# Kernel tuning notes

Hardware: AMD Instinct MI355X
Metric: run time of the kernel (lower is better)

The kernel has to match this reference:

```python
import jax, jax.numpy as jnp
import numpy as np

EPS = 1e-5

def conv3d(x, w, b):
    y = jax.lax.conv_general_dilated(x, w, (1, 1, 1), [(1, 1), (1, 1), (1, 1)],
                                     dimension_numbers=('NCDHW', 'OIDHW', 'NCDHW'))
    return y + b[None, :, None, None, None]

def batchnorm(x, g, b):
    # training-mode BN: biased batch statistics over (N, D, H, W)
    m = jnp.mean(x, axis=(0, 2, 3, 4), keepdims=True)
    v = jnp.mean((x - m) ** 2, axis=(0, 2, 3, 4), keepdims=True)
    return (x - m) * jax.lax.rsqrt(v + EPS) * g[None, :, None, None, None] + b[None, :, None, None, None]

def deform_conv3d(x, offset, w, b):
    # x: (B,C,D,H,W); offset: (B, 3*27, D,H,W); w: (O,C,3,3,3)
    B, C, D, H, W = x.shape
    N = 27
    xp = jnp.pad(x, ((0, 0), (0, 0), (1, 1), (1, 1), (1, 1)))
    Dp, Hp, Wp = D + 2, H + 2, W + 2
    off = offset.reshape(B, 3, N, D, H, W)
    kk = jnp.arange(3, dtype=x.dtype) - 1.0  # kernel taps -1,0,1
    kd, kh, kw = [a.reshape(-1) for a in jnp.meshgrid(kk, kk, kk, indexing='ij')]
    # sampling positions in padded coords: p0 (=out idx + pad) + kernel tap + learned offset
    pd = jnp.clip((jnp.arange(D, dtype=x.dtype) + 1.0)[None, None, :, None, None]
                  + kd[None, :, None, None, None] + off[:, 0], 0.0, Dp - 1)
    ph = jnp.clip((jnp.arange(H, dtype=x.dtype) + 1.0)[None, None, None, :, None]
                  + kh[None, :, None, None, None] + off[:, 1], 0.0, Hp - 1)
    pw = jnp.clip((jnp.arange(W, dtype=x.dtype) + 1.0)[None, None, None, None, :]
                  + kw[None, :, None, None, None] + off[:, 2], 0.0, Wp - 1)
    q0d = jnp.clip(jnp.floor(pd), 0, Dp - 2); td = jnp.clip(pd - q0d, 0.0, 1.0)
    q0h = jnp.clip(jnp.floor(ph), 0, Hp - 2); th = jnp.clip(ph - q0h, 0.0, 1.0)
    q0w = jnp.clip(jnp.floor(pw), 0, Wp - 2); tw = jnp.clip(pw - q0w, 0.0, 1.0)
    q0d = q0d.astype(jnp.int32); q0h = q0h.astype(jnp.int32); q0w = q0w.astype(jnp.int32)
    xf = xp.reshape(B, C, -1)
    acc = jnp.zeros((B, C, N, D, H, W), dtype=x.dtype)
    for i in (0, 1):
        for j in (0, 1):
            for k in (0, 1):
                idx = ((q0d + i) * Hp + (q0h + j)) * Wp + (q0w + k)  # (B,N,D,H,W)
                g = ((td if i else 1.0 - td) * (th if j else 1.0 - th) * (tw if k else 1.0 - tw))
                gath = jnp.take_along_axis(xf, idx.reshape(B, 1, -1), axis=2).reshape(B, C, N, D, H, W)
                acc = acc + g[:, None] * gath
    out = jnp.einsum('bcndhw,ocn->bodhw', acc, w.reshape(w.shape[0], C, N))
    return out + b[None, :, None, None, None]


def setup_inputs() -> dict:
    ks = jax.random.split(jax.random.key(0), 16)
    s = 0.05
    f32 = jnp.float32
    return {
        'x': jax.random.normal(ks[0], (4, 1, 28, 28, 8), f32),
        'c1w': jax.random.normal(ks[1], (32, 1, 3, 3, 3), f32) * s, 'c1b': jnp.zeros((32,), f32),
        'g1': jnp.ones((32,), f32), 'b1': jnp.zeros((32,), f32),
        'c2w': jax.random.normal(ks[2], (64, 32, 3, 3, 3), f32) * s, 'c2b': jnp.zeros((64,), f32),
        'g2': jnp.ones((64,), f32), 'b2': jnp.zeros((64,), f32),
        'c3w': jax.random.normal(ks[3], (128, 64, 3, 3, 3), f32) * s, 'c3b': jnp.zeros((128,), f32),
        'g3': jnp.ones((128,), f32), 'b3': jnp.zeros((128,), f32),
        'ow': jax.random.normal(ks[4], (81, 128, 3, 3, 3), f32) * s, 'ob': jnp.zeros((81,), f32),
        'dw': jax.random.normal(ks[5], (128, 128, 3, 3, 3), f32) * s, 'db': jnp.zeros((128,), f32),
        'g4': jnp.ones((128,), f32), 'b4': jnp.zeros((128,), f32),
        'fcw': jax.random.normal(ks[6], (10, 128), f32) * s, 'fcb': jnp.zeros((10,), f32),
    }


def reference(x, c1w, c1b, g1, b1, c2w, c2b, g2, b2, c3w, c3b, g3, b3,
              ow, ob, dw, db, g4, b4, fcw, fcb):
    h = batchnorm(jax.nn.relu(conv3d(x, c1w, c1b)), g1, b1)
    h = batchnorm(jax.nn.relu(conv3d(h, c2w, c2b)), g2, b2)
    h = batchnorm(jax.nn.relu(conv3d(h, c3w, c3b)), g3, b3)
    offsets = conv3d(h, ow, ob)
    h = batchnorm(jax.nn.relu(deform_conv3d(h, offsets, dw, db)), g4, b4)
    pooled = jnp.mean(h, axis=(2, 3, 4))  # avg_pool over full (28,28,d) extent
    logits = pooled @ fcw.T + fcb
    return jax.nn.log_softmax(logits, axis=1), offsets
```

## Files before the change

kernel.cpp:

```cpp
#include <hip/hip_runtime.h>
#include <hip/hip_bf16.h>
#include <math.h>

#define BB 4
#define SP 6272
#define NSP 25088
#define EPS 1e-5f

typedef unsigned short u16;
typedef __attribute__((ext_vector_type(8))) short v8s;
typedef __attribute__((ext_vector_type(4))) float v4f;

__device__ __forceinline__ u16 f2b(float f) {
    unsigned u = __float_as_uint(f);
    return (u16)((u + 0x7fffu + ((u >> 16) & 1u)) >> 16);
}
__device__ __forceinline__ float b2f(u16 s) {
    return __uint_as_float(((unsigned)s) << 16);
}
__device__ __forceinline__ float b2f_lo(unsigned x) { return __uint_as_float(x << 16); }
__device__ __forceinline__ float b2f_hi(unsigned x) { return __uint_as_float(x & 0xffff0000u); }
__device__ __forceinline__ unsigned pk2(float a, float b) {
    __hip_bfloat162 h = __float22bfloat162_rn(make_float2(a, b));
    unsigned u;
    __builtin_memcpy(&u, &h, 4);
    return u;
}

__global__ __launch_bounds__(256) void prepack_all(const float* __restrict__ c2w,
        const float* __restrict__ c3w, const float* __restrict__ ow,
        const float* __restrict__ dw, u16* __restrict__ wpk2,
        u16* __restrict__ wpk3, u16* __restrict__ wpko, u16* __restrict__ dwa,
        float* __restrict__ ws0, const float* __restrict__ X,
        const float* __restrict__ Wt, const float* __restrict__ c1b,
        u16* __restrict__ Ybf, float* __restrict__ P1s, float* __restrict__ P1q)
{
    int bx = blockIdx.x;
    int tid = threadIdx.x;

    if (bx >= 4544) {
        const int OT = 16;
        __shared__ float red[4][32];
        int c = bx - 4544;
        int xblk = c % 104;
        int o0 = (c / 104) * OT;
        int sblk = (xblk & 7) * 13 + (xblk >> 3);
        if (sblk >= 98) return;
        int t = tid;
        int s = sblk * 256 + t;
        int b = s / SP;
        int sp = s - b * SP;
        int d = sp / 224;
        int r = sp - d * 224;
        int h = r >> 3;
        int w = r & 7;

        float mdh[9]; int odh[9];
        #pragma unroll
        for (int i = 0; i < 3; i++) {
            int dd = d + i - 1;
            float md = ((unsigned)dd < 28u) ? 1.f : 0.f;
            int ddc = min(max(dd, 0), 27);
            #pragma unroll
            for (int j = 0; j < 3; j++) {
                int hh = h + j - 1;
                float mh = ((unsigned)hh < 28u) ? 1.f : 0.f;
                int hhc = min(max(hh, 0), 27);
                mdh[i * 3 + j] = md * mh;
                odh[i * 3 + j] = ddc * 224 + hhc * 8 + w;
            }
        }
        float mw0 = (w > 0) ? 1.f : 0.f;
        float mw2 = (w < 7) ? 1.f : 0.f;

        float acc[OT];
        #pragma unroll
        for (int oo = 0; oo < OT; oo++) acc[oo] = c1b[o0 + oo];

        const float* xc = X + (size_t)b * SP;
        #pragma unroll
        for (int t9 = 0; t9 < 9; t9++) {
            float x0 = xc[odh[t9]];
            float m = mdh[t9];
            float xm = __shfl_up(x0, 1, 64) * (m * mw0);
            float xz = x0 * m;
            float xp = __shfl_down(x0, 1, 64) * (m * mw2);
            #pragma unroll
            for (int oo = 0; oo < OT; oo++) {
                const float* wp = Wt + (size_t)(o0 + oo) * 27 + t9 * 3;
                acc[oo] = fmaf(xm, wp[0], acc[oo]);
                acc[oo] = fmaf(xz, wp[1], acc[oo]);
                acc[oo] = fmaf(xp, wp[2], acc[oo]);
            }
        }
        float sv[OT];
        #pragma unroll
        for (int oo = 0; oo < OT; oo++) sv[oo] = fmaxf(acc[oo], 0.f);

        unsigned pk[8];
        #pragma unroll
        for (int j = 0; j < 8; j++) pk[j] = pk2(sv[2 * j], sv[2 * j + 1]);
        u16* row = Ybf + (size_t)(b * SP + sp) * 32 + o0;
        *(uint4*)(row)     = make_uint4(pk[0], pk[1], pk[2], pk[3]);
        *(uint4*)(row + 8) = make_uint4(pk[4], pk[5], pk[6], pk[7]);

        int l = t & 63, wvv = t >> 6;
        #pragma unroll
        for (int oo = 0; oo < OT; oo++) {
            float ss = sv[oo], qv = ss * ss;
            #pragma unroll
            for (int m = 1; m < 64; m <<= 1) {
                ss += __shfl_xor(ss, m, 64);
                qv += __shfl_xor(qv, m, 64);
            }
            if (l == 0) { red[wvv][oo] = ss; red[wvv][16 + oo] = qv; }
        }
        __syncthreads();
        if (t < 32) {
            float tot = red[0][t] + red[1][t] + red[2][t] + red[3][t];
            if (t < 16) P1s[sblk * 32 + o0 + t] = tot;
            else        P1q[sblk * 32 + o0 + (t - 16)] = tot;
        }
        return;
    }

    if (bx >= 4536) {
        int i = (bx - 4536) * 256 + tid;
        if (i < 2048) ws0[i] = 0.f;
        return;
    }
    int idx = bx * 256 + tid;
    if (idx < 55296) {
        int i = idx;
        int j = i & 7, r = (i >> 3) & 15, q = (i >> 7) & 3;
        int ot = (i >> 9) & 3, t = i >> 11;
        int o = ot * 16 + r, c = q * 8 + j;
        wpk2[i] = f2b(c2w[((size_t)o * 32 + c) * 27 + t]);
    } else if (idx < 276480) {
        int i = idx - 55296;
        int j = i & 7, r = (i >> 3) & 15, q = (i >> 7) & 3;
        int ch = (i >> 9) & 1, ot = (i >> 10) & 7, t = i >> 13;
        int o = ot * 16 + r, c = ch * 32 + q * 8 + j;
        wpk3[i] = f2b(c3w[((size_t)o * 64 + c) * 27 + t]);
    } else if (idx < 718848) {
        int i = idx - 276480;
        int j = i & 7, r = (i >> 3) & 15, q = (i >> 7) & 3;
        int ch = (i >> 9) & 3, ot = (i >> 11) & 7, t = i >> 14;
        int o = ot * 16 + r, c = ch * 32 + q * 8 + j;
        wpko[i] = f2b((o < 81) ? ow[((size_t)o * 128 + c) * 27 + t] : 0.f);
    } else {
        int i = idx - 718848;
        int j = i & 7, r = (i >> 3) & 15, q = (i >> 7) & 3;
        int kc = (i >> 9) & 3, ot = (i >> 11) & 7, n = i >> 14;
        int o = ot * 16 + r, c = kc * 32 + q * 8 + j;
        dwa[i] = f2b(dw[((size_t)o * 128 + c) * 27 + n]);
    }
}

template<int CIN, int OPAD, bool OFFOUT, bool BNIN, bool WIDE, bool PARTIN, bool BNTAIL>
__global__ __launch_bounds__(256) __attribute__((amdgpu_waves_per_eu(1, 4)))
void conv_mfma(const u16* __restrict__ X, const u16* __restrict__ Wpk,
               const float* __restrict__ bias, u16* __restrict__ Ybf,
               float* __restrict__ offs, float* __restrict__ s_sum,
               float* __restrict__ s_sq, const float* __restrict__ in_sum,
               const float* __restrict__ in_sq, const float* __restrict__ in_g,
               const float* __restrict__ in_b)
{
    const int HS = CIN + 8;
    const int NOT = OPAD / 16;
    const int NC = CIN / 32;
    __shared__ u16 xs[160 * HS];
    __shared__ float scin[BNIN ? CIN : 1], shin[BNIN ? CIN : 1];

    int tid = threadIdx.x;
    int fid = blockIdx.x;
    int g = (fid & 7) * 98 + (fid >> 3);
    int b = g / 196;
    int rem = g - b * 196;
    int d0 = (rem / 14) * 2, h0 = (rem % 14) * 2;

    if (BNIN) {
        if (PARTIN) {
            __shared__ float ps[8][32], pq[8][32];
            int ch = tid & 31, ck = tid >> 5;
            float s = 0.f, qq = 0.f;
            for (int k = ck; k < 98; k += 8) {
                s  += in_sum[k * 32 + ch];
                qq += in_sq[k * 32 + ch];
            }
            ps[ck][ch] = s; pq[ck][ch] = qq;
            __syncthreads();
            if (tid < CIN) {
                float m = 0.f, vq = 0.f;
                #pragma unroll
                for (int k2 = 0; k2 < 8; k2++) { m += ps[k2][tid]; vq += pq[k2][tid]; }
                m *= (1.f / NSP);
                vq = vq * (1.f / NSP) - m * m;
                float sc = in_g[tid] * rsqrtf(vq + EPS);
                scin[tid] = sc;
                shin[tid] = in_b[tid] - m * sc;
            }
            __syncthreads();
        } else {
            if (tid < CIN) {
                float m = in_sum[tid] * (1.f / NSP);
                float v = in_sq[tid] * (1.f / NSP) - m * m;
                float sc = in_g[tid] * rsqrtf(v + EPS);
                scin[tid] = sc;
                shin[tid] = in_b[tid] - m * sc;
            }
            __syncthreads();
        }
    }

    if (BNTAIL && fid >= 784) {
        int idx = (fid - 784) * 256 + tid;
        uint4 v = ((const uint4*)X)[idx];
        int cb = (idx & (CIN / 8 - 1)) * 8;
        float f0 = b2f_lo(v.x) * scin[cb]     + shin[cb];
        float f1 = b2f_hi(v.x) * scin[cb + 1] + shin[cb + 1];
        float f2 = b2f_lo(v.y) * scin[cb + 2] + shin[cb + 2];
        float f3 = b2f_hi(v.y) * scin[cb + 3] + shin[cb + 3];
        float f4 = b2f_lo(v.z) * scin[cb + 4] + shin[cb + 4];
        float f5 = b2f_hi(v.z) * scin[cb + 5] + shin[cb + 5];
        float f6 = b2f_lo(v.w) * scin[cb + 6] + shin[cb + 6];
        float f7 = b2f_hi(v.w) * scin[cb + 7] + shin[cb + 7];
        uint4 pk;
        pk.x = pk2(f0, f1); pk.y = pk2(f2, f3);
        pk.z = pk2(f4, f5); pk.w = pk2(f6, f7);
        ((uint4*)Ybf)[idx] = pk;
        return;
    }

    const int NCH = CIN / 8;
    for (int idx = tid; idx < 160 * NCH; idx += 256) {
        int pos = idx / NCH, ch = idx - pos * NCH;
        int dz = pos / 40, r2 = pos - dz * 40;
        int hz = r2 / 10, wz = r2 - hz * 10;
        int dd = d0 + dz - 1, hh = h0 + hz - 1, ww = wz - 1;
        uint4 val = make_uint4(0, 0, 0, 0);
        if ((unsigned)dd < 28u && (unsigned)hh < 28u && (unsigned)ww < 8u) {
            val = *(const uint4*)(X + ((size_t)(b * SP + dd * 224 + hh * 8 + ww) * CIN + ch * 8));
            if (BNIN) {
                int cb = ch * 8;
                float f0 = b2f_lo(val.x) * scin[cb]     + shin[cb];
                float f1 = b2f_hi(val.x) * scin[cb + 1] + shin[cb + 1];
                float f2 = b2f_lo(val.y) * scin[cb + 2] + shin[cb + 2];
                float f3 = b2f_hi(val.y) * scin[cb + 3] + shin[cb + 3];
                float f4 = b2f_lo(val.z) * scin[cb + 4] + shin[cb + 4];
                float f5 = b2f_hi(val.z) * scin[cb + 5] + shin[cb + 5];
                float f6 = b2f_lo(val.w) * scin[cb + 6] + shin[cb + 6];
                float f7 = b2f_hi(val.w) * scin[cb + 7] + shin[cb + 7];
                val.x = pk2(f0, f1); val.y = pk2(f2, f3);
                val.z = pk2(f4, f5); val.w = pk2(f6, f7);
            }
        }
        *(uint4*)(xs + pos * HS + ch * 8) = val;
    }
    __syncthreads();

    int l = tid & 63, wv = tid >> 6;
    int q = l >> 4, r = l & 15;
    int hl = r >> 3, wl = r & 7;

    if (OFFOUT) {
        int dl = wv >> 1;
        int ot0 = (wv & 1) * 3;
        const u16* ap = xs + ((4 + hl + 1) * 10 + wl + 1) * HS + 8 * q + dl * 40 * HS;
        v4f acc[3];
        acc[0] = (v4f){0.f,0.f,0.f,0.f};
        acc[1] = (v4f){0.f,0.f,0.f,0.f};
        acc[2] = (v4f){0.f,0.f,0.f,0.f};
        #pragma unroll
        for (int t = 0; t < 27; t++) {
            const int koff = ((t / 9) - 1) * 40 + (((t / 3) % 3) - 1) * 10 + (t % 3) - 1;
            const u16* wt = Wpk + ((size_t)(t * NOT + ot0) * NC << 9) + l * 8;
            #pragma unroll
            for (int ch = 0; ch < NC; ch++) {
                v8s a0 = *(const v8s*)(ap + koff * HS + ch * 32);
                v8s b0 = *(const v8s*)(wt + ch * 512);
                v8s b1 = *(const v8s*)(wt + (NC + ch) * 512);
                v8s b2 = *(const v8s*)(wt + (2 * NC + ch) * 512);
                acc[0] = __builtin_amdgcn_mfma_f32_16x16x32_bf16(a0, b0, acc[0], 0, 0, 0);
                acc[1] = __builtin_amdgcn_mfma_f32_16x16x32_bf16(a0, b1, acc[1], 0, 0, 0);
                acc[2] = __builtin_amdgcn_mfma_f32_16x16x32_bf16(a0, b2, acc[2], 0, 0, 0);
            }
        }
        int o0 = ot0 * 16 + r;
        #pragma unroll
        for (int j = 0; j < 3; j++) {
            int o = o0 + 16 * j;
            if (o < 81) {
                float bo = bias[o];
                #pragma unroll
                for (int rg = 0; rg < 4; rg++) {
                    int rowl = q * 4 + rg;
                    int sp = (d0 + dl) * 224 + (h0 + (rowl >> 3)) * 8 + (rowl & 7);
                    offs[((size_t)(b * 81 + o)) * SP + sp] = acc[j][rg] + bo;
                }
            }
        }
        return;
    }

    const u16* a0p = xs + ((4 + hl + 1) * 10 + wl + 1) * HS + 8 * q;
    const u16* a1p = a0p + 40 * HS;

    if (WIDE) {
        v4f acc[2][2];
        acc[0][0] = (v4f){0.f,0.f,0.f,0.f}; acc[0][1] = (v4f){0.f,0.f,0.f,0.f};
        acc[1][0] = (v4f){0.f,0.f,0.f,0.f}; acc[1][1] = (v4f){0.f,0.f,0.f,0.f};
        #pragma unroll
        for (int t = 0; t < 27; t++) {
            const int koff = ((t / 9) - 1) * 40 + (((t / 3) % 3) - 1) * 10 + (t % 3) - 1;
            const u16* wt  = Wpk + ((size_t)(t * NOT + wv) * NC << 9) + l * 8;
            const u16* wt2 = wt + (size_t)4 * NC * 512;
            #pragma unroll
            for (int ch = 0; ch < NC; ch++) {
                v8s a0 = *(const v8s*)(a0p + koff * HS + ch * 32);
                v8s a1 = *(const v8s*)(a1p + koff * HS + ch * 32);
                v8s b0 = *(const v8s*)(wt + ch * 512);
                v8s b1 = *(const v8s*)(wt2 + ch * 512);
                acc[0][0] = __builtin_amdgcn_mfma_f32_16x16x32_bf16(a0, b0, acc[0][0], 0, 0, 0);
                acc[0][1] = __builtin_amdgcn_mfma_f32_16x16x32_bf16(a1, b0, acc[0][1], 0, 0, 0);
                acc[1][0] = __builtin_amdgcn_mfma_f32_16x16x32_bf16(a0, b1, acc[1][0], 0, 0, 0);
                acc[1][1] = __builtin_amdgcn_mfma_f32_16x16x32_bf16(a1, b1, acc[1][1], 0, 0, 0);
            }
        }
        #pragma unroll
        for (int oti = 0; oti < 2; oti++) {
            int o_base = wv * 16 + oti * 64;
            int oo = o_base + r;
            float bo = bias[oo];
            float rs = 0.f, rq = 0.f;
            #pragma unroll
            for (int s2 = 0; s2 < 2; s2++) {
                v4f A = acc[oti][s2];
                #pragma unroll
                for (int rg = 0; rg < 4; rg++) {
                    int rowl = q * 4 + rg;
                    int sp = (d0 + s2) * 224 + (h0 + (rowl >> 3)) * 8 + (rowl & 7);
                    float v = fmaxf(A[rg] + bo, 0.f);
                    Ybf[(size_t)(b * SP + sp) * OPAD + oo] = f2b(v);
                    rs += v; rq += v * v;
                }
            }
            rs += __shfl_xor(rs, 16, 64); rs += __shfl_xor(rs, 32, 64);
            rq += __shfl_xor(rq, 16, 64); rq += __shfl_xor(rq, 32, 64);
            if (l < 16) { atomicAdd(&s_sum[o_base + l], rs); atomicAdd(&s_sq[o_base + l], rq); }
        }
        return;
    }

    int o_base = blockIdx.y * 64 + wv * 16;
    int o = o_base + r;
    int otg = o_base >> 4;

    v4f acc0 = {0.f, 0.f, 0.f, 0.f}, acc1 = {0.f, 0.f, 0.f, 0.f};
    #pragma unroll
    for (int t = 0; t < 27; t++) {
        const int koff = ((t / 9) - 1) * 40 + (((t / 3) % 3) - 1) * 10 + (t % 3) - 1;
        const u16* wt = Wpk + ((size_t)(t * NOT + otg) * NC << 9) + l * 8;
        #pragma unroll
        for (int ch = 0; ch < NC; ch++) {
            v8s a0 = *(const v8s*)(a0p + koff * HS + ch * 32);
            v8s a1 = *(const v8s*)(a1p + koff * HS + ch * 32);
            v8s bf = *(const v8s*)(wt + ch * 512);
            acc0 = __builtin_amdgcn_mfma_f32_16x16x32_bf16(a0, bf, acc0, 0, 0, 0);
            acc1 = __builtin_amdgcn_mfma_f32_16x16x32_bf16(a1, bf, acc1, 0, 0, 0);
        }
    }

    {
        float bo = bias[o];
        float rs = 0.f, rq = 0.f;
        #pragma unroll
        for (int s2 = 0; s2 < 2; s2++) {
            v4f A = s2 ? acc1 : acc0;
            #pragma unroll
            for (int rg = 0; rg < 4; rg++) {
                int rowl = q * 4 + rg;
                int sp = (d0 + s2) * 224 + (h0 + (rowl >> 3)) * 8 + (rowl & 7);
                float v = fmaxf(A[rg] + bo, 0.f);
                Ybf[(size_t)(b * SP + sp) * OPAD + o] = f2b(v);
                rs += v; rq += v * v;
            }
        }
        rs += __shfl_xor(rs, 16, 64); rs += __shfl_xor(rs, 32, 64);
        rq += __shfl_xor(rq, 16, 64); rq += __shfl_xor(rq, 32, 64);
        if (l < 16) { atomicAdd(&s_sum[o_base + l], rs); atomicAdd(&s_sq[o_base + l], rq); }
    }
}

__global__ __launch_bounds__(256) __attribute__((amdgpu_waves_per_eu(1, 4)))
void deform_pool(const u16* __restrict__ Ht, const float* __restrict__ OFF,
                 const u16* __restrict__ Wa, const float* __restrict__ db,
                 float* __restrict__ pooledraw, float* __restrict__ sumsq4)
{
    __shared__ float offs_lds[81 * 32];
    __shared__ int ig_s[2][32][8][2];
    __shared__ u16 Vb[2][32][136];
    __shared__ float reds[128], redq[128];

    int fid = blockIdx.x;
    int xcd = fid & 7;
    int local = fid >> 3;
    if (local >= 98) return;
    int b = xcd >> 1;
    int d = (xcd & 1) * 14 + local / 7;
    int h0 = (local % 7) * 4;

    int t = threadIdx.x;
    if (t < 128) { reds[t] = 0.f; redq[t] = 0.f; }

    int gp = t >> 3, gcr = t & 7;
    int glh = gp >> 3, gw = gp & 7, gh = h0 + glh;
    int co = t & 15, pg = t >> 4;
    int l = t & 63, wv = t >> 6;
    int q = l >> 4, r = l & 15;

    v4f acc[2][2];
    acc[0][0] = (v4f){0.f,0.f,0.f,0.f}; acc[0][1] = (v4f){0.f,0.f,0.f,0.f};
    acc[1][0] = (v4f){0.f,0.f,0.f,0.f}; acc[1][1] = (v4f){0.f,0.f,0.f,0.f};

    const u16* hb = Ht + (size_t)b * SP * 128;

    for (int i = t; i < 2592; i += 256) {
        int ch = i >> 5, p = i & 31;
        offs_lds[i] = OFF[(size_t)b * 81 * SP + (size_t)ch * SP
                          + d * 224 + (h0 + (p >> 3)) * 8 + (p & 7)];
    }

    auto GEOM = [&](int n, int tap) {
        int kd = n / 9 - 1, kh = (n / 3) % 3 - 1, kw = n % 3 - 1;
        float od  = offs_lds[n * 32 + gp];
        float oh  = offs_lds[(27 + n) * 32 + gp];
        float owv = offs_lds[(54 + n) * 32 + gp];
        float pd = fminf(fmaxf((float)(d + 1 + kd) + od, 0.f), 29.f);
        float ph = fminf(fmaxf((float)(gh + 1 + kh) + oh, 0.f), 29.f);
        float pw = fminf(fmaxf((float)(gw + 1 + kw) + owv, 0.f), 9.f);
        float qd = fminf(floorf(pd), 28.f);
        float qh = fminf(floorf(ph), 28.f);
        float qw = fminf(floorf(pw), 8.f);
        float td = fminf(pd - qd, 1.f);
        float th = fminf(ph - qh, 1.f);
        float tw = fminf(pw - qw, 1.f);
        int iqd = (int)qd - 1, iqh = (int)qh - 1, iqw = (int)qw - 1;
        int i = gcr >> 2, j = (gcr >> 1) & 1, k = gcr & 1;
        int du = iqd + i, hu = iqh + j, wu = iqw + k;
        bool val = (unsigned)du < 28u && (unsigned)hu < 28u && (unsigned)wu < 8u;
        float gg = (i ? td : 1.f - td) * (j ? th : 1.f - th) * (k ? tw : 1.f - tw);
        ig_s[tap][gp][gcr][0] = val ? (du * 224 + hu * 8 + wu) : 0;
        ig_s[tap][gp][gcr][1] = __float_as_int(val ? gg : 0.f);
    };

    auto SAMPLE = [&](int tap) {
        #pragma unroll
        for (int pp = 0; pp < 2; pp++) {
            int p = pg * 2 + pp;
            float va[8] = {0.f,0.f,0.f,0.f,0.f,0.f,0.f,0.f};
            #pragma unroll
            for (int cr = 0; cr < 8; cr++) {
                int2 pr = *(const int2*)&ig_s[tap][p][cr][0];
                float gg = __int_as_float(pr.y);
                uint4 xv = *(const uint4*)(hb + (size_t)pr.x * 128 + co * 8);
                va[0] = fmaf(gg, b2f_lo(xv.x), va[0]);
                va[1] = fmaf(gg, b2f_hi(xv.x), va[1]);
                va[2] = fmaf(gg, b2f_lo(xv.y), va[2]);
                va[3] = fmaf(gg, b2f_hi(xv.y), va[3]);
                va[4] = fmaf(gg, b2f_lo(xv.z), va[4]);
                va[5] = fmaf(gg, b2f_hi(xv.z), va[5]);
                va[6] = fmaf(gg, b2f_lo(xv.w), va[6]);
                va[7] = fmaf(gg, b2f_hi(xv.w), va[7]);
            }
            uint4 pk;
            pk.x = pk2(va[0], va[1]); pk.y = pk2(va[2], va[3]);
            pk.z = pk2(va[4], va[5]); pk.w = pk2(va[6], va[7]);
            *(uint4*)&Vb[tap][p][co * 8] = pk;
        }
    };

    auto MFMA_TAP = [&](int n, int tap) {
        const u16* wn = Wa + (size_t)n * 16384;
        #pragma unroll
        for (int oti = 0; oti < 2; oti++) {
            int ot = wv * 2 + oti;
            #pragma unroll
            for (int kc = 0; kc < 4; kc++) {
                v8s af = *(const v8s*)(wn + ((((ot * 4 + kc) * 4 + q) * 16 + r) * 8));
                v8s bf0 = *(const v8s*)&Vb[tap][r][kc * 32 + q * 8];
                v8s bf1 = *(const v8s*)&Vb[tap][16 + r][kc * 32 + q * 8];
                acc[oti][0] = __builtin_amdgcn_mfma_f32_16x16x32_bf16(af, bf0, acc[oti][0], 0, 0, 0);
                acc[oti][1] = __builtin_amdgcn_mfma_f32_16x16x32_bf16(af, bf1, acc[oti][1], 0, 0, 0);
            }
        }
    };

    for (int it = 0; it < 14; it++) {
        int n0 = it * 2, n1 = n0 + 1;
        bool two = (n1 < 27);
        __syncthreads();
        GEOM(n0, 0);
        if (two) GEOM(n1, 1);
        __syncthreads();
        SAMPLE(0);
        if (two) SAMPLE(1);
        __syncthreads();
        MFMA_TAP(n0, 0);
        if (two) MFMA_TAP(n1, 1);
    }

    #pragma unroll
    for (int oti = 0; oti < 2; oti++) {
        #pragma unroll
        for (int rg = 0; rg < 4; rg++) {
            int o = (wv * 2 + oti) * 16 + q * 4 + rg;
            float bo = db[o];
            float v0 = fmaxf(acc[oti][0][rg] + bo, 0.f);
            float v1 = fmaxf(acc[oti][1][rg] + bo, 0.f);
            float s = v0 + v1, qq = v0 * v0 + v1 * v1;
            s += __shfl_xor(s, 1, 64);  qq += __shfl_xor(qq, 1, 64);
            s += __shfl_xor(s, 2, 64);  qq += __shfl_xor(qq, 2, 64);
            s += __shfl_xor(s, 4, 64);  qq += __shfl_xor(qq, 4, 64);
            s += __shfl_xor(s, 8, 64);  qq += __shfl_xor(qq, 8, 64);
            if (r == 0) { atomicAdd(&reds[o], s); atomicAdd(&redq[o], qq); }
        }
    }
    __syncthreads();
    if (t < 128) {
        atomicAdd(&pooledraw[b * 128 + t], reds[t]);
        atomicAdd(&sumsq4[t], redq[t]);
    }
}

__global__ __launch_bounds__(256) void final_head_emit(const float* __restrict__ pooledraw,
        const float* __restrict__ sumsq4, const float* __restrict__ g4,
        const float* __restrict__ b4, const float* __restrict__ fcw,
        const float* __restrict__ fcb, float* __restrict__ out)
{
    int t = threadIdx.x;
    __shared__ float pooled_s[4][128];
    __shared__ float logits[4][10];
    if (t < 128) {
        float s0 = pooledraw[t], s1 = pooledraw[128 + t];
        float s2 = pooledraw[256 + t], s3 = pooledraw[384 + t];
        float tot = s0 + s1 + s2 + s3;
        float m  = tot * (1.f / NSP);
        float v  = sumsq4[t] * (1.f / NSP) - m * m;
        float sc = g4[t] * rsqrtf(v + EPS);
        float sh = b4[t] - m * sc;
        pooled_s[0][t] = s0 * (1.f / SP) * sc + sh;
        pooled_s[1][t] = s1 * (1.f / SP) * sc + sh;
        pooled_s[2][t] = s2 * (1.f / SP) * sc + sh;
        pooled_s[3][t] = s3 * (1.f / SP) * sc + sh;
    }
    __syncthreads();
    if (t < 40) {
        int b = t / 10, j = t % 10;
        float l = fcb[j];
        for (int c = 0; c < 128; c++) l = fmaf(pooled_s[b][c], fcw[j * 128 + c], l);
        logits[b][j] = l;
    }
    __syncthreads();
    if (t < 4) {
        float mx = -1e30f;
        for (int j = 0; j < 10; j++) mx = fmaxf(mx, logits[t][j]);
        float se = 0.f;
        for (int j = 0; j < 10; j++) se += expf(logits[t][j] - mx);
        float lse = mx + logf(se);
        for (int j = 0; j < 10; j++) out[t * 10 + j] = logits[t][j] - lse;
    }
}

extern "C" void kernel_launch(void* const* d_in, const int* in_sizes, int n_in,
                              void* d_out, int out_size, void* d_ws, size_t ws_size,
                              hipStream_t stream)
{
    (void)in_sizes; (void)n_in; (void)out_size; (void)ws_size;
    const float* x   = (const float*)d_in[0];
    const float* c1w = (const float*)d_in[1];
    const float* c1b = (const float*)d_in[2];
    const float* g1  = (const float*)d_in[3];
    const float* b1  = (const float*)d_in[4];
    const float* c2w = (const float*)d_in[5];
    const float* c2b = (const float*)d_in[6];
    const float* g2  = (const float*)d_in[7];
    const float* b2  = (const float*)d_in[8];
    const float* c3w = (const float*)d_in[9];
    const float* c3b = (const float*)d_in[10];
    const float* g3  = (const float*)d_in[11];
    const float* b3  = (const float*)d_in[12];
    const float* ow  = (const float*)d_in[13];
    const float* ob  = (const float*)d_in[14];
    const float* dw  = (const float*)d_in[15];
    const float* db  = (const float*)d_in[16];
    const float* g4  = (const float*)d_in[17];
    const float* b4  = (const float*)d_in[18];
    const float* fcw = (const float*)d_in[19];
    const float* fcb = (const float*)d_in[20];

    float* ws = (float*)d_ws;
    float* S2 = ws + 64,  *Q2 = ws + 128;
    float* S3 = ws + 192, *Q3 = ws + 320;
    float* PO = ws + 448;
    float* Q4 = ws + 960;
    float* P1s = ws + 4096;
    float* P1q = ws + 7232;
    u16* y1bf = (u16*)(ws + 16384);
    u16* y2bf = y1bf + 802816;
    u16* y3bf = y2bf + 1605632;
    u16* x3bf = y3bf + 3211264;
    u16* wpk2 = x3bf + 3211264;
    u16* wpk3 = wpk2 + 55296;
    u16* wpko = wpk3 + 221184;
    u16* dwa  = wpko + 442368;

    float* outf = (float*)d_out;
    float* offp = outf + 40;

    prepack_all<<<4752, 256, 0, stream>>>(c2w, c3w, ow, dw, wpk2, wpk3, wpko, dwa,
                                          ws, x, c1w, c1b, y1bf, P1s, P1q);

    conv_mfma<32, 64, false, true, false, true, false><<<784, 256, 0, stream>>>(
        y1bf, wpk2, c2b, y2bf, nullptr, S2, Q2, P1s, P1q, g1, b1);

    conv_mfma<64, 128, false, true, true, false, false><<<784, 256, 0, stream>>>(
        y2bf, wpk3, c3b, y3bf, nullptr, S3, Q3, S2, Q2, g2, b2);

    conv_mfma<128, 128, true, true, false, false, true><<<2352, 256, 0, stream>>>(
        y3bf, wpko, ob, x3bf, offp, nullptr, nullptr, S3, Q3, g3, b3);

    deform_pool<<<800, 256, 0, stream>>>(x3bf, offp, dwa, db, PO, Q4);

    final_head_emit<<<1, 256, 0, stream>>>(PO, Q4, g4, b4, fcw, fcb, outf);
}
```

Measured before the change: 341.8 us.

## Split conv output channels across a second grid dimension to raise block count

Adds a SPLIT2 path in which each block computes only half of the conv2 output-channel tiles, selected by blockIdx.y. Each wave handles one depth slice and one output tile, with a single accumulator, and fuses bias, ReLU, the bf16 store and the BN statistics atomics. conv2 now launches a 784x2 grid. conv3 drops its WIDE path and also gets a 784x2 grid, and the waves-per-EU hint is raised from 4 to 8. The goal is more blocks and higher occupancy, at the cost of staging the input tile twice and issuing more atomics. Correctness of conv3 depends on whether the non-WIDE path already partitions its work by blockIdx.y; if it does not, that layer computes everything twice and double-counts the BN statistics.

Result: slower. 364.0 us (+6.5%).

```diff
diff --git a/kernel.cpp b/kernel.cpp
--- a/kernel.cpp
+++ b/kernel.cpp
@@ -157,8 +157,9 @@
     }
 }
 
-template<int CIN, int OPAD, bool OFFOUT, bool BNIN, bool WIDE, bool PARTIN, bool BNTAIL>
-__global__ __launch_bounds__(256) __attribute__((amdgpu_waves_per_eu(1, 4)))
+template<int CIN, int OPAD, bool OFFOUT, bool BNIN, bool WIDE, bool PARTIN,
+         bool BNTAIL, bool SPLIT2>
+__global__ __launch_bounds__(256) __attribute__((amdgpu_waves_per_eu(1, 8)))
 void conv_mfma(const u16* __restrict__ X, const u16* __restrict__ Wpk,
                const float* __restrict__ bias, u16* __restrict__ Ybf,
                float* __restrict__ offs, float* __restrict__ s_sum,
@@ -300,6 +301,39 @@
                 }
             }
         }
+        return;
+    }
+
+    if (SPLIT2) {
+        int dl = wv >> 1;
+        int ot = blockIdx.y * 2 + (wv & 1);
+        const u16* ap = xs + ((4 + hl + 1) * 10 + wl + 1) * HS + 8 * q + dl * 40 * HS;
+        v4f acc = {0.f, 0.f, 0.f, 0.f};
+        #pragma unroll
+        for (int t = 0; t < 27; t++) {
+            const int koff = ((t / 9) - 1) * 40 + (((t / 3) % 3) - 1) * 10 + (t % 3) - 1;
+            const u16* wt = Wpk + ((size_t)(t * NOT + ot) * NC << 9) + l * 8;
+            #pragma unroll
+            for (int ch = 0; ch < NC; ch++) {
+                v8s a0 = *(const v8s*)(ap + koff * HS + ch * 32);
+                v8s bf = *(const v8s*)(wt + ch * 512);
+                acc = __builtin_amdgcn_mfma_f32_16x16x32_bf16(a0, bf, acc, 0, 0, 0);
+            }
+        }
+        int o = ot * 16 + r;
+        float bo = bias[o];
+        float rs = 0.f, rq = 0.f;
+        #pragma unroll
+        for (int rg = 0; rg < 4; rg++) {
+            int rowl = q * 4 + rg;
+            int sp = (d0 + dl) * 224 + (h0 + (rowl >> 3)) * 8 + (rowl & 7);
+            float v = fmaxf(acc[rg] + bo, 0.f);
+            Ybf[(size_t)(b * SP + sp) * OPAD + o] = f2b(v);
+            rs += v; rq += v * v;
+        }
+        rs += __shfl_xor(rs, 16, 64); rs += __shfl_xor(rs, 32, 64);
+        rq += __shfl_xor(rq, 16, 64); rq += __shfl_xor(rq, 32, 64);
+        if (l < 16) { atomicAdd(&s_sum[ot * 16 + l], rs); atomicAdd(&s_sq[ot * 16 + l], rq); }
         return;
     }
 
@@ -621,13 +655,16 @@
     prepack_all<<<4752, 256, 0, stream>>>(c2w, c3w, ow, dw, wpk2, wpk3, wpko, dwa,
                                           ws, x, c1w, c1b, y1bf, P1s, P1q);
 
-    conv_mfma<32, 64, false, true, false, true, false><<<784, 256, 0, stream>>>(
+    conv_mfma<32, 64, false, true, false, true, false, true>
+        <<<dim3(784, 2), 256, 0, stream>>>(
         y1bf, wpk2, c2b, y2bf, nullptr, S2, Q2, P1s, P1q, g1, b1);
 
-    conv_mfma<64, 128, false, true, true, false, false><<<784, 256, 0, stream>>>(
+    conv_mfma<64, 128, false, true, false, false, false, false>
+        <<<dim3(784, 2), 256, 0, stream>>>(
         y2bf, wpk3, c3b, y3bf, nullptr, S3, Q3, S2, Q2, g2, b2);
 
-    conv_mfma<128, 128, true, true, false, false, true><<<2352, 256, 0, stream>>>(
+    conv_mfma<128, 128, true, true, false, false, true, false>
+        <<<2352, 256, 0, stream>>>(
         y3bf, wpko, ob, x3bf, offp, nullptr, nullptr, S3, Q3, g3, b3);
 
     deform_pool<<<800, 256, 0, stream>>>(x3bf, offp, dwa, db, PO, Q4);
```
